# Optimization experiments

Hardware: AMD Instinct MI355X
Metric: run time of the kernel (lower is better)

The kernel has to match this reference:

```python
import jax, jax.numpy as jnp
import numpy as np

B, N, D = 4, 1024, 256
HEADS, LVLS, PTS, KSAMP = 8, 1, 4, 10
HF, WF, C = 200, 200, 256
HD = D // HEADS


def setup_inputs() -> dict:
    key = jax.random.key(0)
    ks = jax.random.split(key, 16)
    s = 0.02
    return {
        "query_embed": jax.random.normal(ks[0], (B, N, D), jnp.float32),
        # ctrl points in metric BEV coords (roughly inside pc_range)
        "ctrl_points": jax.random.normal(ks[1], (B, N, 4, 2), jnp.float32) * 30.0,
        "bev_features": jax.random.normal(ks[2], (B, C, HF, WF), jnp.float32),
        "spatial_shapes": jnp.array([[HF, WF]], jnp.int32),
        "pc_range": jnp.array([-51.2, -51.2, -5.0, 51.2, 51.2, 3.0], jnp.float32),
        # query_proj
        "W_q": jax.random.normal(ks[3], (D, D), jnp.float32) * s,
        "b_q": jnp.zeros((D,), jnp.float32),
        # MSDeformAttn.value_proj
        "W_val": jax.random.normal(ks[4], (D, D), jnp.float32) * s,
        "b_val": jnp.zeros((D,), jnp.float32),
        # MSDeformAttn.sampling_offsets  (D -> heads*levels*points*2)
        "W_off": jax.random.normal(ks[5], (D, HEADS * LVLS * PTS * 2), jnp.float32) * s,
        "b_off": jax.random.normal(ks[6], (HEADS * LVLS * PTS * 2,), jnp.float32) * 2.0,
        # MSDeformAttn.attention_weights (D -> heads*levels*points)
        "W_attn": jax.random.normal(ks[7], (D, HEADS * LVLS * PTS), jnp.float32) * s,
        "b_attn": jnp.zeros((HEADS * LVLS * PTS,), jnp.float32),
        # MSDeformAttn.output_proj
        "W_do": jax.random.normal(ks[8], (D, D), jnp.float32) * s,
        "b_do": jnp.zeros((D,), jnp.float32),
        # BezierDeformableAttention.output_proj
        "W_out": jax.random.normal(ks[9], (D, D), jnp.float32) * s,
        "b_out": jnp.zeros((D,), jnp.float32),
    }


def _forward(query_embed, ctrl_points, bev_features, pc_range,
             W_q, b_q, W_val, b_val, W_off, b_off, W_attn, b_attn,
             W_do, b_do, W_out, b_out):
    Bb, Nn = ctrl_points.shape[:2]
    _, Cc, Hh, Ww = bev_features.shape

    # ---- cubic Bezier interpolation: (B,N,4,2) -> (B,N,K,2) ----
    t = jnp.linspace(0.0, 1.0, KSAMP, dtype=query_embed.dtype)
    u = 1.0 - t
    coeff = jnp.stack([u ** 3, 3 * u ** 2 * t, 3 * u * t ** 2, t ** 3], axis=-1)  # (K,4)
    dense = jnp.einsum('kc,bncd->bnkd', coeff, ctrl_points)  # (B,N,K,2)

    # ---- normalize to [0,1] by pc_range, clamp ----
    lo = pc_range[:2]
    span = pc_range[3:5] - pc_range[:2]
    ref = jnp.clip((dense - lo) / span, 0.01, 0.99)  # (B,N,K,2)
    ref_center = ref.mean(axis=2)  # (B,N,2) -- center of the Bezier curve

    # ---- projections ----
    query = query_embed @ W_q + b_q  # (B,N,D)
    value = (bev_features.reshape(Bb, Cc, Hh * Ww).transpose(0, 2, 1) @ W_val + b_val)
    value = value.reshape(Bb, Hh * Ww, HEADS, HD)  # (B,HW,h,hd)

    offsets = (query @ W_off + b_off).reshape(Bb, Nn, HEADS, LVLS, PTS, 2)
    attn = (query @ W_attn + b_attn).reshape(Bb, Nn, HEADS, LVLS * PTS)
    attn = jax.nn.softmax(attn, axis=-1)  # (B,N,h,P)

    # sampling locations: ref (B,N,1(levels),2) + offsets/[W,H]
    norm = jnp.array([Ww, Hh], dtype=query.dtype)  # offset_normalizer (x=W, y=H)
    loc = ref_center[:, :, None, None, None, :] + offsets / norm  # (B,N,h,1,P,2)
    grid = 2.0 * loc[:, :, :, 0] - 1.0  # single level -> (B,N,h,P,2)

    # ---- bilinear grid_sample, align_corners=False, zero padding ----
    BH = Bb * HEADS
    val = value.transpose(0, 2, 3, 1).reshape(BH, HD, Hh * Ww)  # (BH,hd,HW)
    g = grid.transpose(0, 2, 1, 3, 4).reshape(BH, Nn, PTS, 2)  # (BH,N,P,2)
    x = (g[..., 0] + 1.0) * 0.5 * Ww - 0.5
    y = (g[..., 1] + 1.0) * 0.5 * Hh - 0.5
    x0 = jnp.floor(x).astype(jnp.int32); x1 = x0 + 1
    y0 = jnp.floor(y).astype(jnp.int32); y1 = y0 + 1
    wx = (x - x0).astype(val.dtype); wy = (y - y0).astype(val.dtype)

    def gather(yi, xi):
        valid = ((yi >= 0) & (yi < Hh) & (xi >= 0) & (xi < Ww))
        idx = jnp.clip(yi, 0, Hh - 1) * Ww + jnp.clip(xi, 0, Ww - 1)  # (BH,N,P)
        gv = jnp.take_along_axis(val, idx.reshape(BH, 1, Nn * PTS), axis=2)
        gv = gv.reshape(BH, HD, Nn, PTS)
        return gv * valid.astype(val.dtype)[:, None, :, :]

    sampled = (gather(y0, x0) * ((1 - wx) * (1 - wy))[:, None]
               + gather(y0, x1) * (wx * (1 - wy))[:, None]
               + gather(y1, x0) * ((1 - wx) * wy)[:, None]
               + gather(y1, x1) * (wx * wy)[:, None])  # (BH,hd,N,P)

    w = attn.transpose(0, 2, 1, 3).reshape(BH, 1, Nn, PTS)
    out = (sampled * w).sum(axis=-1)  # (BH,hd,N)
    out = out.reshape(Bb, HEADS * HD, Nn).transpose(0, 2, 1)  # (B,N,D)

    # mmcv MultiScaleDeformableAttention: output_proj + residual (identity = query)
    msda = out @ W_do + b_do + query
    return msda @ W_out + b_out


def reference(query_embed, ctrl_points, bev_features, spatial_shapes, pc_range,
              W_q, b_q, W_val, b_val, W_off, b_off, W_attn, b_attn,
              W_do, b_do, W_out, b_out):
    # spatial_shapes is recomputed from bev_features inside the torch module; unused here
    del spatial_shapes
    return _forward(query_embed, ctrl_points, bev_features, pc_range,
                    W_q, b_q, W_val, b_val, W_off, b_off, W_attn, b_attn,
                    W_do, b_do, W_out, b_out)
```

## Files before the change

kernel.cpp:

```cpp
#include <hip/hip_runtime.h>
#include <hip/hip_bf16.h>

#define BB 4
#define NN 1024
#define DD 256
#define NHEADS 8
#define NPTS 4
#define NKSAMP 10
#define HHF 200
#define WWF 200
#define HWF (HHF*WWF)

typedef __hip_bfloat16 bf16;

__device__ __forceinline__ float ldf(const float* p, size_t i){ return p[i]; }
__device__ __forceinline__ float ldf(const bf16*  p, size_t i){ return __bfloat162float(p[i]); }

__device__ __forceinline__ unsigned short f2bf(float f){
    unsigned u = __float_as_uint(f);
    return (unsigned short)((u + 0x7FFFu + ((u >> 16) & 1u)) >> 16);
}
__device__ __forceinline__ void load_bf16x8(const unsigned short* p, float* v){
    int4 t = *reinterpret_cast<const int4*>(p);
    unsigned q0 = (unsigned)t.x, q1 = (unsigned)t.y, q2 = (unsigned)t.z, q3 = (unsigned)t.w;
    v[0] = __uint_as_float(q0 << 16); v[1] = __uint_as_float(q0 & 0xFFFF0000u);
    v[2] = __uint_as_float(q1 << 16); v[3] = __uint_as_float(q1 & 0xFFFF0000u);
    v[4] = __uint_as_float(q2 << 16); v[5] = __uint_as_float(q2 & 0xFFFF0000u);
    v[6] = __uint_as_float(q3 << 16); v[7] = __uint_as_float(q3 & 0xFFFF0000u);
}
__device__ __forceinline__ void store_bf16x8(unsigned short* p, const float* v){
    int4 t;
    t.x = (int)((unsigned)f2bf(v[0]) | ((unsigned)f2bf(v[1]) << 16));
    t.y = (int)((unsigned)f2bf(v[2]) | ((unsigned)f2bf(v[3]) << 16));
    t.z = (int)((unsigned)f2bf(v[4]) | ((unsigned)f2bf(v[5]) << 16));
    t.w = (int)((unsigned)f2bf(v[6]) | ((unsigned)f2bf(v[7]) << 16));
    *reinterpret_cast<int4*>(p) = t;
}

__global__ void detect_kernel(const unsigned* __restrict__ pc_bits, int* __restrict__ flag){
    if (threadIdx.x == 0 && blockIdx.x == 0)
        *flag = (pc_bits[0] == 0xC24CCCCDu) ? 0 : 1;
}

template<typename T, int WANT>
__global__ __launch_bounds__(256) void transpose_kernel(const T* __restrict__ bev,
                                                        unsigned short* __restrict__ bevT,
                                                        const int* __restrict__ flag){
    if (*flag != WANT) return;
    __shared__ unsigned short tile[32][33];
    int b  = blockIdx.z;
    int c0 = blockIdx.y * 32;
    int p0 = blockIdx.x * 32;
    int tx = threadIdx.x & 31;
    int ty = threadIdx.x >> 5;
    const T* src = bev + (size_t)b * DD * HWF;
    #pragma unroll
    for (int i = 0; i < 4; i++){
        int c = c0 + ty + i*8;
        tile[ty + i*8][tx] = f2bf(ldf(src, (size_t)c * HWF + p0 + tx));
    }
    __syncthreads();
    unsigned short* dst = bevT + (size_t)b * HWF * DD;
    #pragma unroll
    for (int i = 0; i < 4; i++){
        int p = p0 + ty + i*8;
        dst[(size_t)p * DD + c0 + tx] = tile[tx][ty + i*8];
    }
}

template<int NT, int NM, bool ABF16, bool HEADSLICE, bool WSBIAS, bool RES, int WANT>
__global__ __launch_bounds__(256) void gemm_kernel(
    const void* __restrict__ Av, int lda,
    const float* __restrict__ B, int ldb,
    const float* __restrict__ bias,
    const float* __restrict__ wsb,
    const float* __restrict__ res,
    float* __restrict__ C, int ldc,
    const int* __restrict__ flag)
{
    if (*flag != WANT) return;
    __shared__ float As[256][68];
    const int n0  = blockIdx.x * NT;
    const int m0  = blockIdx.y * 64;
    const int tid = threadIdx.x;
    const int koff = HEADSLICE ? (n0 >> 5) * 256 : 0;

    if (ABF16){
        const unsigned short* A = (const unsigned short*)Av;
        int r  = tid >> 2;
        int kb = (tid & 3) * 8;
        #pragma unroll
        for (int kk = 0; kk < 8; kk++){
            int k = kb + kk*32;
            float v[8];
            load_bf16x8(A + (size_t)(m0 + r)*lda + koff + k, v);
            #pragma unroll
            for (int t = 0; t < 8; t++) As[k + t][r] = v[t];
        }
    } else {
        const float* A = (const float*)Av;
        int r  = tid >> 2;
        int kb = (tid & 3) * 4;
        #pragma unroll
        for (int kk = 0; kk < 16; kk++){
            int k = kb + kk*16;
            float4 v = *reinterpret_cast<const float4*>(A + (size_t)(m0 + r)*lda + k);
            As[k+0][r] = v.x; As[k+1][r] = v.y; As[k+2][r] = v.z; As[k+3][r] = v.w;
        }
    }
    __syncthreads();

    const int ti = tid & 15;
    const int tj = tid >> 4;
    float acc[4][NM];
    #pragma unroll
    for (int i = 0; i < 4; i++)
        #pragma unroll
        for (int j = 0; j < NM; j++) acc[i][j] = 0.f;

    const float* Bp = B + n0 + tj*NM;
    #pragma unroll 4
    for (int c = 0; c < 256; c++){
        float4 a = *reinterpret_cast<const float4*>(&As[c][ti*4]);
        float av[4] = {a.x, a.y, a.z, a.w};
        float bv[NM];
        if (NM == 4){
            float4 b4 = *reinterpret_cast<const float4*>(Bp + (size_t)c*ldb);
            bv[0] = b4.x; bv[1] = b4.y; bv[2] = b4.z; bv[3] = b4.w;
        } else {
            float2 b2 = *reinterpret_cast<const float2*>(Bp + (size_t)c*ldb);
            bv[0] = b2.x; bv[1] = b2.y;
        }
        #pragma unroll
        for (int i = 0; i < 4; i++)
            #pragma unroll
            for (int j = 0; j < NM; j++) acc[i][j] += av[i] * bv[j];
    }

    #pragma unroll
    for (int i = 0; i < 4; i++){
        int row = m0 + ti*4 + i;
        #pragma unroll
        for (int j = 0; j < NM; j++){
            int n = n0 + tj*NM + j;
            float bvv = bias[n];
            float v = acc[i][j] + (WSBIAS ? wsb[(size_t)row*8 + (n0 >> 5)]*bvv : bvv);
            if (RES) v += res[(size_t)row*256 + n];
            C[(size_t)row*ldc + n] = v;
        }
    }
}

template<int WANT>
__global__ __launch_bounds__(256) void coords_kernel(
    const float* __restrict__ ctrl, const float* __restrict__ pc,
    const float* __restrict__ oa,
    float* __restrict__ coords,
    float* __restrict__ wsb,
    const int* __restrict__ flag)
{
    if (*flag != WANT) return;
    const int m0 = blockIdx.x * 32;
    const int r  = threadIdx.x >> 3;
    const int h  = threadIdx.x & 7;
    const int m  = m0 + r;

    float cx[4], cy[4];
    #pragma unroll
    for (int i = 0; i < 4; i++){
        cx[i] = ctrl[(size_t)m*8 + i*2 + 0];
        cy[i] = ctrl[(size_t)m*8 + i*2 + 1];
    }
    float lox = pc[0], loy = pc[1];
    float spx = pc[3] - lox, spy = pc[4] - loy;
    float sx = 0.f, sy = 0.f;
    for (int k = 0; k < NKSAMP; k++){
        float t = (float)k / (float)(NKSAMP - 1);
        float u = 1.f - t;
        float c0 = u*u*u, c1 = 3.f*u*u*t, c2 = 3.f*u*t*t, c3 = t*t*t;
        float dx = c0*cx[0] + c1*cx[1] + c2*cx[2] + c3*cx[3];
        float dy = c0*cy[0] + c1*cy[1] + c2*cy[2] + c3*cy[3];
        float rx = fminf(fmaxf((dx - lox)/spx, 0.01f), 0.99f);
        float ry = fminf(fmaxf((dy - loy)/spy, 0.01f), 0.99f);
        sx += rx; sy += ry;
    }
    float cxp = (sx / (float)NKSAMP) * (float)WWF - 0.5f;
    float cyp = (sy / (float)NKSAMP) * (float)HHF - 0.5f;

    const float* row = oa + (size_t)m*96;
    float a0 = row[64 + h*4 + 0], a1 = row[64 + h*4 + 1];
    float a2 = row[64 + h*4 + 2], a3 = row[64 + h*4 + 3];
    float mx = fmaxf(fmaxf(a0, a1), fmaxf(a2, a3));
    float e0 = __expf(a0 - mx), e1 = __expf(a1 - mx);
    float e2 = __expf(a2 - mx), e3 = __expf(a3 - mx);
    float inv = 1.f / (e0 + e1 + e2 + e3);
    float wp[4] = {e0*inv, e1*inv, e2*inv, e3*inv};

    float* cp = coords + ((size_t)m*8 + h)*12;
    float wsum = 0.f;
    #pragma unroll
    for (int p = 0; p < 4; p++){
        float x = cxp + row[h*8 + p*2 + 0];
        float y = cyp + row[h*8 + p*2 + 1];
        cp[p*3 + 0] = x; cp[p*3 + 1] = y; cp[p*3 + 2] = wp[p];
        float fx = floorf(x), fy = floorf(y);
        int x0 = (int)fx, y0 = (int)fy;
        float wx = x - fx, wy = y - fy;
        bool vx0 = (unsigned)x0 < WWF, vx1 = (unsigned)(x0+1) < WWF;
        bool vy0 = (unsigned)y0 < HHF, vy1 = (unsigned)(y0+1) < HHF;
        float w = wp[p];
        if (vy0 && vx0) wsum += w*(1.f-wx)*(1.f-wy);
        if (vy0 && vx1) wsum += w*wx*(1.f-wy);
        if (vy1 && vx0) wsum += w*(1.f-wx)*wy;
        if (vy1 && vx1) wsum += w*wx*wy;
    }
    wsb[(size_t)m*8 + h] = wsum;
}

template<bool TRANS, int WANT>
__global__ __launch_bounds__(256) void gather_kernel(
    const unsigned short* __restrict__ bevT,
    const float* __restrict__ bev,
    const float* __restrict__ coords,
    unsigned short* __restrict__ g,
    const int* __restrict__ flag)
{
    if (*flag != WANT) return;
    const int m0  = blockIdx.x * 4;
    const int b   = m0 >> 10;
    const int sub = threadIdx.x & 31;
    const int grp = threadIdx.x >> 5;

    for (int it = 0; it < 4; it++){
        int rh = it*8 + grp;
        int m  = m0 + (rh >> 3);
        int h  = rh & 7;
        float acc[8] = {0.f,0.f,0.f,0.f,0.f,0.f,0.f,0.f};
        const float* cp = coords + ((size_t)m*8 + h)*12;

        #pragma unroll
        for (int p = 0; p < 4; p++){
            float x = cp[p*3+0], y = cp[p*3+1], w = cp[p*3+2];
            float fx = floorf(x), fy = floorf(y);
            int x0 = (int)fx, y0 = (int)fy;
            float wx = x - fx, wy = y - fy;
            int   xs[4] = {x0, x0+1, x0,   x0+1};
            int   ys[4] = {y0, y0,   y0+1, y0+1};
            float ws4[4] = {w*(1.f-wx)*(1.f-wy), w*wx*(1.f-wy), w*(1.f-wx)*wy, w*wx*wy};
            #pragma unroll
            for (int cidx = 0; cidx < 4; cidx++){
                int xi = xs[cidx], yi = ys[cidx];
                if ((unsigned)xi < WWF && (unsigned)yi < HHF){
                    float wgt = ws4[cidx];
                    if (TRANS){
                        const unsigned short* rowp =
                            bevT + (((size_t)b*HWF + yi*WWF + xi)*DD + sub*8);
                        float v[8]; load_bf16x8(rowp, v);
                        #pragma unroll
                        for (int i = 0; i < 8; i++) acc[i] += wgt * v[i];
                    } else {
                        size_t base = ((size_t)b*DD + sub*8)*HWF + (size_t)(yi*WWF + xi);
                        #pragma unroll
                        for (int i = 0; i < 8; i++) acc[i] += wgt * bev[base + (size_t)i*HWF];
                    }
                }
            }
        }
        store_bf16x8(g + ((size_t)m*2048 + h*256 + sub*8), acc);
    }
}

template<typename T, bool TRANS, int WANT>
__global__ __launch_bounds__(256) void monolith_kernel(
    const T* __restrict__ qe, const T* __restrict__ ctrl,
    const T* __restrict__ bev, const bf16* __restrict__ bevT,
    const T* __restrict__ pc,
    const T* __restrict__ Wq, const T* __restrict__ bq,
    const T* __restrict__ Wval, const T* __restrict__ bval,
    const T* __restrict__ Woff, const T* __restrict__ boff,
    const T* __restrict__ Wattn, const T* __restrict__ battn,
    const T* __restrict__ Wdo, const T* __restrict__ bdo,
    const T* __restrict__ Wout, const T* __restrict__ bout,
    float* __restrict__ out, const int* __restrict__ flag)
{
    if (*flag != WANT) return;
    __shared__ float qe_s[4][256];
    __shared__ float q_s[4][256];
    __shared__ float oa_s[4][96];
    __shared__ float cen_s[4][2];
    __shared__ int   sx0_s[4][32];
    __shared__ int   sy0_s[4][32];
    __shared__ float swx_s[4][32];
    __shared__ float swy_s[4][32];
    __shared__ float sww_s[4][32];
    __shared__ float ws_s[4][8];
    __shared__ float g_s[4][2048];
    __shared__ float t_s[4][256];

    const int m0  = blockIdx.x * 4;
    const int b   = m0 >> 10;
    const int tid = threadIdx.x;

    for (int i = tid; i < 4*256; i += 256){
        int r = i >> 8, c = i & 255;
        qe_s[r][c] = ldf(qe, (size_t)(m0 + r)*256 + c);
    }
    if (tid < 4){
        int r = tid;
        float cx[4], cy[4];
        #pragma unroll
        for (int i = 0; i < 4; i++){
            cx[i] = ldf(ctrl, (size_t)(m0+r)*8 + i*2 + 0);
            cy[i] = ldf(ctrl, (size_t)(m0+r)*8 + i*2 + 1);
        }
        float lox = ldf(pc,0), loy = ldf(pc,1);
        float spx = ldf(pc,3) - lox, spy = ldf(pc,4) - loy;
        float sx = 0.f, sy = 0.f;
        for (int k = 0; k < NKSAMP; k++){
            float t = (float)k / (float)(NKSAMP - 1);
            float u = 1.f - t;
            float c0 = u*u*u, c1 = 3.f*u*u*t, c2 = 3.f*u*t*t, c3 = t*t*t;
            float dx = c0*cx[0] + c1*cx[1] + c2*cx[2] + c3*cx[3];
            float dy = c0*cy[0] + c1*cy[1] + c2*cy[2] + c3*cy[3];
            float rx = fminf(fmaxf((dx - lox)/spx, 0.01f), 0.99f);
            float ry = fminf(fmaxf((dy - loy)/spy, 0.01f), 0.99f);
            sx += rx; sy += ry;
        }
        cen_s[r][0] = sx / (float)NKSAMP;
        cen_s[r][1] = sy / (float)NKSAMP;
    }
    __syncthreads();

    {
        const int j = tid;
        float acc[4] = {0.f, 0.f, 0.f, 0.f};
        for (int c = 0; c < 256; c++){
            float w = ldf(Wq, (size_t)c*256 + j);
            #pragma unroll
            for (int r = 0; r < 4; r++) acc[r] += qe_s[r][c] * w;
        }
        float bias = ldf(bq, j);
        #pragma unroll
        for (int r = 0; r < 4; r++) q_s[r][j] = acc[r] + bias;
    }
    __syncthreads();

    for (int idx = tid; idx < 4*96; idx += 256){
        int r = idx / 96, col = idx % 96;
        float acc = 0.f;
        if (col < 64){
            for (int c = 0; c < 256; c++) acc += q_s[r][c] * ldf(Woff, (size_t)c*64 + col);
            acc += ldf(boff, col);
        } else {
            int cc = col - 64;
            for (int c = 0; c < 256; c++) acc += q_s[r][c] * ldf(Wattn, (size_t)c*32 + cc);
            acc += ldf(battn, cc);
        }
        oa_s[r][col] = acc;
    }
    __syncthreads();

    if (tid < 32){
        int r = tid >> 3, h = tid & 7;
        float a0 = oa_s[r][64 + h*4 + 0], a1 = oa_s[r][64 + h*4 + 1];
        float a2 = oa_s[r][64 + h*4 + 2], a3 = oa_s[r][64 + h*4 + 3];
        float mx = fmaxf(fmaxf(a0, a1), fmaxf(a2, a3));
        float e0 = __expf(a0 - mx), e1 = __expf(a1 - mx);
        float e2 = __expf(a2 - mx), e3 = __expf(a3 - mx);
        float inv = 1.f / (e0 + e1 + e2 + e3);
        float wp[4] = {e0*inv, e1*inv, e2*inv, e3*inv};
        float cxp = cen_s[r][0] * (float)WWF - 0.5f;
        float cyp = cen_s[r][1] * (float)HHF - 0.5f;
        float wsum = 0.f;
        #pragma unroll
        for (int p = 0; p < 4; p++){
            float x = cxp + oa_s[r][h*8 + p*2 + 0];
            float y = cyp + oa_s[r][h*8 + p*2 + 1];
            float fx = floorf(x), fy = floorf(y);
            int x0 = (int)fx, y0 = (int)fy;
            float wx = x - fx, wy = y - fy;
            int s = h*4 + p;
            sx0_s[r][s] = x0; sy0_s[r][s] = y0;
            swx_s[r][s] = wx; swy_s[r][s] = wy;
            sww_s[r][s] = wp[p];
            bool vx0 = (unsigned)x0 < WWF, vx1 = (unsigned)(x0+1) < WWF;
            bool vy0 = (unsigned)y0 < HHF, vy1 = (unsigned)(y0+1) < HHF;
            float w = wp[p];
            if (vy0 && vx0) wsum += w*(1.f-wx)*(1.f-wy);
            if (vy0 && vx1) wsum += w*wx*(1.f-wy);
            if (vy1 && vx0) wsum += w*(1.f-wx)*wy;
            if (vy1 && vx1) wsum += w*wx*wy;
        }
        ws_s[r][h] = wsum;
    }
    __syncthreads();

    {
        const int c = tid;
        const bf16* baseT = bevT + (size_t)b * HWF * DD;
        const T*    baseR = bev  + (size_t)b * DD * HWF;
        for (int r = 0; r < 4; r++){
            #pragma unroll
            for (int h = 0; h < 8; h++){
                float acc = 0.f;
                #pragma unroll
                for (int p = 0; p < 4; p++){
                    int s = h*4 + p;
                    int x0 = sx0_s[r][s], y0 = sy0_s[r][s];
                    float wx = swx_s[r][s], wy = swy_s[r][s], w = sww_s[r][s];
                    float w00 = w*(1.f-wx)*(1.f-wy);
                    float w01 = w*wx*(1.f-wy);
                    float w10 = w*(1.f-wx)*wy;
                    float w11 = w*wx*wy;
                    bool vy0 = (unsigned)y0 < HHF, vy1 = (unsigned)(y0+1) < HHF;
                    bool vx0 = (unsigned)x0 < WWF, vx1 = (unsigned)(x0+1) < WWF;
                    if (vy0){
                        int rowp = y0*WWF + x0;
                        if (vx0) acc += w00 * (TRANS ? __bfloat162float(baseT[(size_t)rowp*DD + c])
                                                     : ldf(baseR, (size_t)c*HWF + rowp));
                        if (vx1) acc += w01 * (TRANS ? __bfloat162float(baseT[(size_t)(rowp+1)*DD + c])
                                                     : ldf(baseR, (size_t)c*HWF + rowp+1));
                    }
                    if (vy1){
                        int rowp = (y0+1)*WWF + x0;
                        if (vx0) acc += w10 * (TRANS ? __bfloat162float(baseT[(size_t)rowp*DD + c])
                                                     : ldf(baseR, (size_t)c*HWF + rowp));
                        if (vx1) acc += w11 * (TRANS ? __bfloat162float(baseT[(size_t)(rowp+1)*DD + c])
                                                     : ldf(baseR, (size_t)c*HWF + rowp+1));
                    }
                }
                g_s[r][h*256 + c] = acc;
            }
        }
    }
    __syncthreads();

    {
        const int j = tid;
        const int h = j >> 5;
        float acc[4] = {0.f, 0.f, 0.f, 0.f};
        for (int c = 0; c < 256; c++){
            float w = ldf(Wval, (size_t)c*256 + j);
            #pragma unroll
            for (int r = 0; r < 4; r++) acc[r] += g_s[r][h*256 + c] * w;
        }
        float bv = ldf(bval, j);
        #pragma unroll
        for (int r = 0; r < 4; r++) t_s[r][j] = acc[r] + ws_s[r][h] * bv;
    }
    __syncthreads();

    {
        const int j = tid;
        float acc[4] = {0.f, 0.f, 0.f, 0.f};
        for (int c = 0; c < 256; c++){
            float w = ldf(Wdo, (size_t)c*256 + j);
            #pragma unroll
            for (int r = 0; r < 4; r++) acc[r] += t_s[r][c] * w;
        }
        __syncthreads();
        float bd = ldf(bdo, j);
        #pragma unroll
        for (int r = 0; r < 4; r++) t_s[r][j] = acc[r] + bd + q_s[r][j];
    }
    __syncthreads();

    {
        const int j = tid;
        float acc[4] = {0.f, 0.f, 0.f, 0.f};
        for (int c = 0; c < 256; c++){
            float w = ldf(Wout, (size_t)c*256 + j);
            #pragma unroll
            for (int r = 0; r < 4; r++) acc[r] += t_s[r][c] * w;
        }
        float bo = ldf(bout, j);
        #pragma unroll
        for (int r = 0; r < 4; r++)
            out[(size_t)(m0+r)*256 + j] = acc[r] + bo;
    }
}

template<typename T, bool TRANS, int WANT>
static void launch_monolith(void* const* d_in, const bf16* bevT, float* out,
                            const int* flag, hipStream_t stream)
{
    monolith_kernel<T, TRANS, WANT><<<dim3(BB*NN/4), 256, 0, stream>>>(
        (const T*)d_in[0], (const T*)d_in[1], (const T*)d_in[2], bevT,
        (const T*)d_in[4],
        (const T*)d_in[5], (const T*)d_in[6], (const T*)d_in[7], (const T*)d_in[8],
        (const T*)d_in[9], (const T*)d_in[10], (const T*)d_in[11], (const T*)d_in[12],
        (const T*)d_in[13], (const T*)d_in[14], (const T*)d_in[15], (const T*)d_in[16],
        out, flag);
}

extern "C" void kernel_launch(void* const* d_in, const int* in_sizes, int n_in,
                              void* d_out, int out_size, void* d_ws, size_t ws_size,
                              hipStream_t stream)
{
    (void)in_sizes; (void)n_in; (void)out_size;
    float* out = (float*)d_out;
    char*  ws  = (char*)d_ws;

    const size_t OF_FLAG = 0;
    const size_t OF_QBUF = 256;
    const size_t OF_OA   = OF_QBUF + (size_t)4096*256*4;
    const size_t OF_CO   = OF_OA   + (size_t)4096*96*4;
    const size_t OF_WSB  = OF_CO   + (size_t)4096*8*48;
    const size_t OF_T1   = OF_WSB  + (size_t)4096*8*4;
    const size_t OF_T2   = OF_T1   + (size_t)4096*256*4;
    const size_t OF_G    = OF_T2   + (size_t)4096*256*4;
    const size_t OF_BT   = OF_G    + (size_t)4096*2048*2;
    const size_t NEED_A  = OF_BT + (size_t)BB*HWF*DD*2;
    const size_t NEED_R4 = 64 + (size_t)BB*HWF*DD*2;
    const size_t NEED_B  = OF_BT;

    int*            flag   = (int*)(ws + OF_FLAG);
    float*          qbuf   = (float*)(ws + OF_QBUF);
    float*          oa     = (float*)(ws + OF_OA);
    float*          coords = (float*)(ws + OF_CO);
    float*          wsb    = (float*)(ws + OF_WSB);
    float*          t1     = (float*)(ws + OF_T1);
    float*          t2     = (float*)(ws + OF_T2);
    unsigned short* g      = (unsigned short*)(ws + OF_G);
    unsigned short* bevT   = (unsigned short*)(ws + OF_BT);

    const float* qe    = (const float*)d_in[0];
    const float* ctrl  = (const float*)d_in[1];
    const float* bev   = (const float*)d_in[2];
    const float* pc    = (const float*)d_in[4];
    const float* Wq    = (const float*)d_in[5];
    const float* bq    = (const float*)d_in[6];
    const float* Wval  = (const float*)d_in[7];
    const float* bval  = (const float*)d_in[8];
    const float* Woff  = (const float*)d_in[9];
    const float* boff  = (const float*)d_in[10];
    const float* Wattn = (const float*)d_in[11];
    const float* battn = (const float*)d_in[12];
    const float* Wdo   = (const float*)d_in[13];
    const float* bdo   = (const float*)d_in[14];
    const float* Wout  = (const float*)d_in[15];
    const float* bout  = (const float*)d_in[16];

    detect_kernel<<<1, 64, 0, stream>>>((const unsigned*)d_in[4], flag);

    if (ws_size >= NEED_A || ws_size >= NEED_B){
        const bool haveT = (ws_size >= NEED_A);

        if (haveT)
            transpose_kernel<float, 0><<<dim3(HWF/32, DD/32, BB), 256, 0, stream>>>(
                bev, bevT, flag);

        gemm_kernel<64,4,false,false,false,false,0><<<dim3(4,64), 256, 0, stream>>>(
            qe, 256, Wq, 256, bq, nullptr, nullptr, qbuf, 256, flag);
        gemm_kernel<64,4,false,false,false,false,0><<<dim3(1,64), 256, 0, stream>>>(
            qbuf, 256, Woff, 64, boff, nullptr, nullptr, oa, 96, flag);
        gemm_kernel<32,2,false,false,false,false,0><<<dim3(1,64), 256, 0, stream>>>(
            qbuf, 256, Wattn, 32, battn, nullptr, nullptr, oa + 64, 96, flag);
        coords_kernel<0><<<dim3(128), 256, 0, stream>>>(ctrl, pc, oa, coords, wsb, flag);
        if (haveT)
            gather_kernel<true, 0><<<dim3(1024), 256, 0, stream>>>(bevT, bev, coords, g, flag);
        else
            gather_kernel<false,0><<<dim3(1024), 256, 0, stream>>>(bevT, bev, coords, g, flag);
        gemm_kernel<32,2,true,true,true,false,0><<<dim3(8,64), 256, 0, stream>>>(
            g, 2048, Wval, 256, bval, wsb, nullptr, t1, 256, flag);
        gemm_kernel<64,4,false,false,false,true,0><<<dim3(4,64), 256, 0, stream>>>(
            t1, 256, Wdo, 256, bdo, nullptr, qbuf, t2, 256, flag);
        gemm_kernel<64,4,false,false,false,false,0><<<dim3(4,64), 256, 0, stream>>>(
            t2, 256, Wout, 256, bout, nullptr, nullptr, out, 256, flag);

        if (haveT){
            transpose_kernel<bf16, 1><<<dim3(HWF/32, DD/32, BB), 256, 0, stream>>>(
                (const bf16*)d_in[2], bevT, flag);
            launch_monolith<bf16, true, 1>(d_in, (const bf16*)bevT, out, flag, stream);
        } else {
            launch_monolith<bf16, false, 1>(d_in, (const bf16*)bevT, out, flag, stream);
        }
    } else if (ws_size >= NEED_R4){
        bf16* bevT4 = (bf16*)(ws + 64);
        transpose_kernel<float, 0><<<dim3(HWF/32, DD/32, BB), 256, 0, stream>>>(
            bev, (unsigned short*)bevT4, flag);
        transpose_kernel<bf16, 1><<<dim3(HWF/32, DD/32, BB), 256, 0, stream>>>(
            (const bf16*)d_in[2], (unsigned short*)bevT4, flag);
        launch_monolith<float, true, 0>(d_in, bevT4, out, flag, stream);
        launch_monolith<bf16,  true, 1>(d_in, bevT4, out, flag, stream);
    } else {
        launch_monolith<float, false, 0>(d_in, (const bf16*)ws, out, flag, stream);
        launch_monolith<bf16,  false, 1>(d_in, (const bf16*)ws, out, flag, stream);
    }
}
```

Baseline: 533.1 us.

## Fuse offset/attention projections with coords kernel and drop the runtime dtype dispatch

Merges the sampling-offset GEMM, the attention-weight GEMM and the coordinate/softmax computation into one kernel that keeps the projection results in shared memory. This removes the intermediate buffer and two launches. It also deletes the flag-based runtime detection and the bf16 fallback path, including the monolith kernel and the flag-gated launches that used to exit early. GEMM epilogue stores become float4/float2 vector writes. In exchange, the fused kernel runs on only 64 blocks, and the code now supports only float32 inputs with the full workspace layout.

```diff
diff --git a/kernel.cpp b/kernel.cpp
--- a/kernel.cpp
+++ b/kernel.cpp
@@ -13,9 +13,6 @@
 
 typedef __hip_bfloat16 bf16;
 
-__device__ __forceinline__ float ldf(const float* p, size_t i){ return p[i]; }
-__device__ __forceinline__ float ldf(const bf16*  p, size_t i){ return __bfloat162float(p[i]); }
-
 __device__ __forceinline__ unsigned short f2bf(float f){
     unsigned u = __float_as_uint(f);
     return (unsigned short)((u + 0x7FFFu + ((u >> 16) & 1u)) >> 16);
@@ -37,27 +34,19 @@
     *reinterpret_cast<int4*>(p) = t;
 }
 
-__global__ void detect_kernel(const unsigned* __restrict__ pc_bits, int* __restrict__ flag){
-    if (threadIdx.x == 0 && blockIdx.x == 0)
-        *flag = (pc_bits[0] == 0xC24CCCCDu) ? 0 : 1;
-}
-
-template<typename T, int WANT>
-__global__ __launch_bounds__(256) void transpose_kernel(const T* __restrict__ bev,
-                                                        unsigned short* __restrict__ bevT,
-                                                        const int* __restrict__ flag){
-    if (*flag != WANT) return;
+__global__ __launch_bounds__(256) void transpose_kernel(const float* __restrict__ bev,
+                                                        unsigned short* __restrict__ bevT){
     __shared__ unsigned short tile[32][33];
     int b  = blockIdx.z;
     int c0 = blockIdx.y * 32;
     int p0 = blockIdx.x * 32;
     int tx = threadIdx.x & 31;
     int ty = threadIdx.x >> 5;
-    const T* src = bev + (size_t)b * DD * HWF;
+    const float* src = bev + (size_t)b * DD * HWF;
     #pragma unroll
     for (int i = 0; i < 4; i++){
         int c = c0 + ty + i*8;
-        tile[ty + i*8][tx] = f2bf(ldf(src, (size_t)c * HWF + p0 + tx));
+        tile[ty + i*8][tx] = f2bf(src[(size_t)c * HWF + p0 + tx]);
     }
     __syncthreads();
     unsigned short* dst = bevT + (size_t)b * HWF * DD;
@@ -68,17 +57,15 @@
     }
 }
 
-template<int NT, int NM, bool ABF16, bool HEADSLICE, bool WSBIAS, bool RES, int WANT>
+template<int NT, int NM, bool ABF16, bool HEADSLICE, bool WSBIAS, bool RES>
 __global__ __launch_bounds__(256) void gemm_kernel(
     const void* __restrict__ Av, int lda,
     const float* __restrict__ B, int ldb,
     const float* __restrict__ bias,
     const float* __restrict__ wsb,
     const float* __restrict__ res,
-    float* __restrict__ C, int ldc,
-    const int* __restrict__ flag)
+    float* __restrict__ C, int ldc)
 {
-    if (*flag != WANT) return;
     __shared__ float As[256][68];
     const int n0  = blockIdx.x * NT;
     const int m0  = blockIdx.y * 64;
@@ -140,92 +127,157 @@
     #pragma unroll
     for (int i = 0; i < 4; i++){
         int row = m0 + ti*4 + i;
-        #pragma unroll
-        for (int j = 0; j < NM; j++){
-            int n = n0 + tj*NM + j;
-            float bvv = bias[n];
-            float v = acc[i][j] + (WSBIAS ? wsb[(size_t)row*8 + (n0 >> 5)]*bvv : bvv);
-            if (RES) v += res[(size_t)row*256 + n];
-            C[(size_t)row*ldc + n] = v;
-        }
-    }
-}
-
-template<int WANT>
-__global__ __launch_bounds__(256) void coords_kernel(
-    const float* __restrict__ ctrl, const float* __restrict__ pc,
-    const float* __restrict__ oa,
+        float wsv = WSBIAS ? wsb[(size_t)row*8 + (n0 >> 5)] : 0.f;
+        if (NM == 4){
+            float4 v; float* vp = (float*)&v;
+            #pragma unroll
+            for (int j = 0; j < 4; j++){
+                int n = n0 + tj*4 + j;
+                float bvv = bias[n];
+                float t = acc[i][j] + (WSBIAS ? wsv*bvv : bvv);
+                if (RES) t += res[(size_t)row*256 + n];
+                vp[j] = t;
+            }
+            *reinterpret_cast<float4*>(&C[(size_t)row*ldc + n0 + tj*4]) = v;
+        } else {
+            float2 v; float* vp = (float*)&v;
+            #pragma unroll
+            for (int j = 0; j < 2; j++){
+                int n = n0 + tj*2 + j;
+                float bvv = bias[n];
+                float t = acc[i][j] + (WSBIAS ? wsv*bvv : bvv);
+                if (RES) t += res[(size_t)row*256 + n];
+                vp[j] = t;
+            }
+            *reinterpret_cast<float2*>(&C[(size_t)row*ldc + n0 + tj*2]) = v;
+        }
+    }
+}
+
+__global__ __launch_bounds__(256) void oacoords_kernel(
+    const float* __restrict__ Q, const float* __restrict__ ctrl, const float* __restrict__ pc,
+    const float* __restrict__ Woff, const float* __restrict__ boff,
+    const float* __restrict__ Wattn, const float* __restrict__ battn,
     float* __restrict__ coords,
-    float* __restrict__ wsb,
-    const int* __restrict__ flag)
+    float* __restrict__ wsb)
 {
-    if (*flag != WANT) return;
-    const int m0 = blockIdx.x * 32;
-    const int r  = threadIdx.x >> 3;
-    const int h  = threadIdx.x & 7;
-    const int m  = m0 + r;
-
-    float cx[4], cy[4];
-    #pragma unroll
-    for (int i = 0; i < 4; i++){
-        cx[i] = ctrl[(size_t)m*8 + i*2 + 0];
-        cy[i] = ctrl[(size_t)m*8 + i*2 + 1];
-    }
-    float lox = pc[0], loy = pc[1];
-    float spx = pc[3] - lox, spy = pc[4] - loy;
-    float sx = 0.f, sy = 0.f;
-    for (int k = 0; k < NKSAMP; k++){
-        float t = (float)k / (float)(NKSAMP - 1);
-        float u = 1.f - t;
-        float c0 = u*u*u, c1 = 3.f*u*u*t, c2 = 3.f*u*t*t, c3 = t*t*t;
-        float dx = c0*cx[0] + c1*cx[1] + c2*cx[2] + c3*cx[3];
-        float dy = c0*cy[0] + c1*cy[1] + c2*cy[2] + c3*cy[3];
-        float rx = fminf(fmaxf((dx - lox)/spx, 0.01f), 0.99f);
-        float ry = fminf(fmaxf((dy - loy)/spy, 0.01f), 0.99f);
-        sx += rx; sy += ry;
-    }
-    float cxp = (sx / (float)NKSAMP) * (float)WWF - 0.5f;
-    float cyp = (sy / (float)NKSAMP) * (float)HHF - 0.5f;
-
-    const float* row = oa + (size_t)m*96;
-    float a0 = row[64 + h*4 + 0], a1 = row[64 + h*4 + 1];
-    float a2 = row[64 + h*4 + 2], a3 = row[64 + h*4 + 3];
-    float mx = fmaxf(fmaxf(a0, a1), fmaxf(a2, a3));
-    float e0 = __expf(a0 - mx), e1 = __expf(a1 - mx);
-    float e2 = __expf(a2 - mx), e3 = __expf(a3 - mx);
-    float inv = 1.f / (e0 + e1 + e2 + e3);
-    float wp[4] = {e0*inv, e1*inv, e2*inv, e3*inv};
-
-    float* cp = coords + ((size_t)m*8 + h)*12;
-    float wsum = 0.f;
-    #pragma unroll
-    for (int p = 0; p < 4; p++){
-        float x = cxp + row[h*8 + p*2 + 0];
-        float y = cyp + row[h*8 + p*2 + 1];
-        cp[p*3 + 0] = x; cp[p*3 + 1] = y; cp[p*3 + 2] = wp[p];
-        float fx = floorf(x), fy = floorf(y);
-        int x0 = (int)fx, y0 = (int)fy;
-        float wx = x - fx, wy = y - fy;
-        bool vx0 = (unsigned)x0 < WWF, vx1 = (unsigned)(x0+1) < WWF;
-        bool vy0 = (unsigned)y0 < HHF, vy1 = (unsigned)(y0+1) < HHF;
-        float w = wp[p];
-        if (vy0 && vx0) wsum += w*(1.f-wx)*(1.f-wy);
-        if (vy0 && vx1) wsum += w*wx*(1.f-wy);
-        if (vy1 && vx0) wsum += w*(1.f-wx)*wy;
-        if (vy1 && vx1) wsum += w*wx*wy;
-    }
-    wsb[(size_t)m*8 + h] = wsum;
-}
-
-template<bool TRANS, int WANT>
+    __shared__ __align__(16) char smem[256*68*4];
+    float (*As)[68] = (float(*)[68])smem;
+    __shared__ float cen_s[64][2];
+    const int m0  = blockIdx.x * 64;
+    const int tid = threadIdx.x;
+
+    {
+        int r  = tid >> 2;
+        int kb = (tid & 3) * 4;
+        #pragma unroll
+        for (int kk = 0; kk < 16; kk++){
+            int k = kb + kk*16;
+            float4 v = *reinterpret_cast<const float4*>(Q + (size_t)(m0 + r)*256 + k);
+            As[k+0][r] = v.x; As[k+1][r] = v.y; As[k+2][r] = v.z; As[k+3][r] = v.w;
+        }
+    }
+    if (tid < 64){
+        int m = m0 + tid;
+        float cx[4], cy[4];
+        #pragma unroll
+        for (int i = 0; i < 4; i++){
+            cx[i] = ctrl[(size_t)m*8 + i*2 + 0];
+            cy[i] = ctrl[(size_t)m*8 + i*2 + 1];
+        }
+        float lox = pc[0], loy = pc[1];
+        float spx = pc[3] - lox, spy = pc[4] - loy;
+        float sx = 0.f, sy = 0.f;
+        for (int k = 0; k < NKSAMP; k++){
+            float t = (float)k / (float)(NKSAMP - 1);
+            float u = 1.f - t;
+            float c0 = u*u*u, c1 = 3.f*u*u*t, c2 = 3.f*u*t*t, c3 = t*t*t;
+            float dx = c0*cx[0] + c1*cx[1] + c2*cx[2] + c3*cx[3];
+            float dy = c0*cy[0] + c1*cy[1] + c2*cy[2] + c3*cy[3];
+            float rx = fminf(fmaxf((dx - lox)/spx, 0.01f), 0.99f);
+            float ry = fminf(fmaxf((dy - loy)/spy, 0.01f), 0.99f);
+            sx += rx; sy += ry;
+        }
+        cen_s[tid][0] = (sx / (float)NKSAMP) * (float)WWF - 0.5f;
+        cen_s[tid][1] = (sy / (float)NKSAMP) * (float)HHF - 0.5f;
+    }
+    __syncthreads();
+
+    const int ti = tid & 15;
+    const int tj = tid >> 4;
+    float ao[4][4], aa[4][2];
+    #pragma unroll
+    for (int i = 0; i < 4; i++){
+        #pragma unroll
+        for (int j = 0; j < 4; j++) ao[i][j] = 0.f;
+        aa[i][0] = 0.f; aa[i][1] = 0.f;
+    }
+    #pragma unroll 4
+    for (int c = 0; c < 256; c++){
+        float4 a = *reinterpret_cast<const float4*>(&As[c][ti*4]);
+        float av[4] = {a.x, a.y, a.z, a.w};
+        float4 bo = *reinterpret_cast<const float4*>(Woff + (size_t)c*64 + tj*4);
+        float2 ba = *reinterpret_cast<const float2*>(Wattn + (size_t)c*32 + tj*2);
+        #pragma unroll
+        for (int i = 0; i < 4; i++){
+            ao[i][0] += av[i]*bo.x; ao[i][1] += av[i]*bo.y;
+            ao[i][2] += av[i]*bo.z; ao[i][3] += av[i]*bo.w;
+            aa[i][0] += av[i]*ba.x; aa[i][1] += av[i]*ba.y;
+        }
+    }
+    __syncthreads();
+    float* oaS = (float*)smem;
+    #pragma unroll
+    for (int i = 0; i < 4; i++){
+        int r = ti*4 + i;
+        #pragma unroll
+        for (int j = 0; j < 4; j++) oaS[r*96 + tj*4 + j] = ao[i][j] + boff[tj*4 + j];
+        oaS[r*96 + 64 + tj*2 + 0] = aa[i][0] + battn[tj*2 + 0];
+        oaS[r*96 + 64 + tj*2 + 1] = aa[i][1] + battn[tj*2 + 1];
+    }
+    __syncthreads();
+
+    for (int idx = tid; idx < 512; idx += 256){
+        int r = idx >> 3, h = idx & 7;
+        int m = m0 + r;
+        const float* row = oaS + r*96;
+        float a0 = row[64 + h*4 + 0], a1 = row[64 + h*4 + 1];
+        float a2 = row[64 + h*4 + 2], a3 = row[64 + h*4 + 3];
+        float mx = fmaxf(fmaxf(a0, a1), fmaxf(a2, a3));
+        float e0 = __expf(a0 - mx), e1 = __expf(a1 - mx);
+        float e2 = __expf(a2 - mx), e3 = __expf(a3 - mx);
+        float inv = 1.f / (e0 + e1 + e2 + e3);
+        float wp[4] = {e0*inv, e1*inv, e2*inv, e3*inv};
+        float cxp = cen_s[r][0], cyp = cen_s[r][1];
+        float* cp = coords + ((size_t)m*8 + h)*12;
+        float wsum = 0.f;
+        #pragma unroll
+        for (int p = 0; p < 4; p++){
+            float x = cxp + row[h*8 + p*2 + 0];
+            float y = cyp + row[h*8 + p*2 + 1];
+            cp[p*3 + 0] = x; cp[p*3 + 1] = y; cp[p*3 + 2] = wp[p];
+            float fx = floorf(x), fy = floorf(y);
+            int x0 = (int)fx, y0 = (int)fy;
+            float wx = x - fx, wy = y - fy;
+            bool vx0 = (unsigned)x0 < WWF, vx1 = (unsigned)(x0+1) < WWF;
+            bool vy0 = (unsigned)y0 < HHF, vy1 = (unsigned)(y0+1) < HHF;
+            float w = wp[p];
+            if (vy0 && vx0) wsum += w*(1.f-wx)*(1.f-wy);
+            if (vy0 && vx1) wsum += w*wx*(1.f-wy);
+            if (vy1 && vx0) wsum += w*(1.f-wx)*wy;
+            if (vy1 && vx1) wsum += w*wx*wy;
+        }
+        wsb[(size_t)m*8 + h] = wsum;
+    }
+}
+
+template<bool TRANS>
 __global__ __launch_bounds__(256) void gather_kernel(
     const unsigned short* __restrict__ bevT,
     const float* __restrict__ bev,
     const float* __restrict__ coords,
-    unsigned short* __restrict__ g,
-    const int* __restrict__ flag)
+    unsigned short* __restrict__ g)
 {
-    if (*flag != WANT) return;
     const int m0  = blockIdx.x * 4;
     const int b   = m0 >> 10;
     const int sub = threadIdx.x & 31;
@@ -244,8 +296,8 @@
             float fx = floorf(x), fy = floorf(y);
             int x0 = (int)fx, y0 = (int)fy;
             float wx = x - fx, wy = y - fy;
-            int   xs[4] = {x0, x0+1, x0,   x0+1};
-            int   ys[4] = {y0, y0,   y0+1, y0+1};
+            int   xs[4]  = {x0, x0+1, x0,   x0+1};
+            int   ys[4]  = {y0, y0,   y0+1, y0+1};
             float ws4[4] = {w*(1.f-wx)*(1.f-wy), w*wx*(1.f-wy), w*(1.f-wx)*wy, w*wx*wy};
             #pragma unroll
             for (int cidx = 0; cidx < 4; cidx++){
@@ -270,229 +322,6 @@
     }
 }
 
-template<typename T, bool TRANS, int WANT>
-__global__ __launch_bounds__(256) void monolith_kernel(
-    const T* __restrict__ qe, const T* __restrict__ ctrl,
-    const T* __restrict__ bev, const bf16* __restrict__ bevT,
-    const T* __restrict__ pc,
-    const T* __restrict__ Wq, const T* __restrict__ bq,
-    const T* __restrict__ Wval, const T* __restrict__ bval,
-    const T* __restrict__ Woff, const T* __restrict__ boff,
-    const T* __restrict__ Wattn, const T* __restrict__ battn,
-    const T* __restrict__ Wdo, const T* __restrict__ bdo,
-    const T* __restrict__ Wout, const T* __restrict__ bout,
-    float* __restrict__ out, const int* __restrict__ flag)
-{
-    if (*flag != WANT) return;
-    __shared__ float qe_s[4][256];
-    __shared__ float q_s[4][256];
-    __shared__ float oa_s[4][96];
-    __shared__ float cen_s[4][2];
-    __shared__ int   sx0_s[4][32];
-    __shared__ int   sy0_s[4][32];
-    __shared__ float swx_s[4][32];
-    __shared__ float swy_s[4][32];
-    __shared__ float sww_s[4][32];
-    __shared__ float ws_s[4][8];
-    __shared__ float g_s[4][2048];
-    __shared__ float t_s[4][256];
-
-    const int m0  = blockIdx.x * 4;
-    const int b   = m0 >> 10;
-    const int tid = threadIdx.x;
-
-    for (int i = tid; i < 4*256; i += 256){
-        int r = i >> 8, c = i & 255;
-        qe_s[r][c] = ldf(qe, (size_t)(m0 + r)*256 + c);
-    }
-    if (tid < 4){
-        int r = tid;
-        float cx[4], cy[4];
-        #pragma unroll
-        for (int i = 0; i < 4; i++){
-            cx[i] = ldf(ctrl, (size_t)(m0+r)*8 + i*2 + 0);
-            cy[i] = ldf(ctrl, (size_t)(m0+r)*8 + i*2 + 1);
-        }
-        float lox = ldf(pc,0), loy = ldf(pc,1);
-        float spx = ldf(pc,3) - lox, spy = ldf(pc,4) - loy;
-        float sx = 0.f, sy = 0.f;
-        for (int k = 0; k < NKSAMP; k++){
-            float t = (float)k / (float)(NKSAMP - 1);
-            float u = 1.f - t;
-            float c0 = u*u*u, c1 = 3.f*u*u*t, c2 = 3.f*u*t*t, c3 = t*t*t;
-            float dx = c0*cx[0] + c1*cx[1] + c2*cx[2] + c3*cx[3];
-            float dy = c0*cy[0] + c1*cy[1] + c2*cy[2] + c3*cy[3];
-            float rx = fminf(fmaxf((dx - lox)/spx, 0.01f), 0.99f);
-            float ry = fminf(fmaxf((dy - loy)/spy, 0.01f), 0.99f);
-            sx += rx; sy += ry;
-        }
-        cen_s[r][0] = sx / (float)NKSAMP;
-        cen_s[r][1] = sy / (float)NKSAMP;
-    }
-    __syncthreads();
-
-    {
-        const int j = tid;
-        float acc[4] = {0.f, 0.f, 0.f, 0.f};
-        for (int c = 0; c < 256; c++){
-            float w = ldf(Wq, (size_t)c*256 + j);
-            #pragma unroll
-            for (int r = 0; r < 4; r++) acc[r] += qe_s[r][c] * w;
-        }
-        float bias = ldf(bq, j);
-        #pragma unroll
-        for (int r = 0; r < 4; r++) q_s[r][j] = acc[r] + bias;
-    }
-    __syncthreads();
-
-    for (int idx = tid; idx < 4*96; idx += 256){
-        int r = idx / 96, col = idx % 96;
-        float acc = 0.f;
-        if (col < 64){
-            for (int c = 0; c < 256; c++) acc += q_s[r][c] * ldf(Woff, (size_t)c*64 + col);
-            acc += ldf(boff, col);
-        } else {
-            int cc = col - 64;
-            for (int c = 0; c < 256; c++) acc += q_s[r][c] * ldf(Wattn, (size_t)c*32 + cc);
-            acc += ldf(battn, cc);
-        }
-        oa_s[r][col] = acc;
-    }
-    __syncthreads();
-
-    if (tid < 32){
-        int r = tid >> 3, h = tid & 7;
-        float a0 = oa_s[r][64 + h*4 + 0], a1 = oa_s[r][64 + h*4 + 1];
-        float a2 = oa_s[r][64 + h*4 + 2], a3 = oa_s[r][64 + h*4 + 3];
-        float mx = fmaxf(fmaxf(a0, a1), fmaxf(a2, a3));
-        float e0 = __expf(a0 - mx), e1 = __expf(a1 - mx);
-        float e2 = __expf(a2 - mx), e3 = __expf(a3 - mx);
-        float inv = 1.f / (e0 + e1 + e2 + e3);
-        float wp[4] = {e0*inv, e1*inv, e2*inv, e3*inv};
-        float cxp = cen_s[r][0] * (float)WWF - 0.5f;
-        float cyp = cen_s[r][1] * (float)HHF - 0.5f;
-        float wsum = 0.f;
-        #pragma unroll
-        for (int p = 0; p < 4; p++){
-            float x = cxp + oa_s[r][h*8 + p*2 + 0];
-            float y = cyp + oa_s[r][h*8 + p*2 + 1];
-            float fx = floorf(x), fy = floorf(y);
-            int x0 = (int)fx, y0 = (int)fy;
-            float wx = x - fx, wy = y - fy;
-            int s = h*4 + p;
-            sx0_s[r][s] = x0; sy0_s[r][s] = y0;
-            swx_s[r][s] = wx; swy_s[r][s] = wy;
-            sww_s[r][s] = wp[p];
-            bool vx0 = (unsigned)x0 < WWF, vx1 = (unsigned)(x0+1) < WWF;
-            bool vy0 = (unsigned)y0 < HHF, vy1 = (unsigned)(y0+1) < HHF;
-            float w = wp[p];
-            if (vy0 && vx0) wsum += w*(1.f-wx)*(1.f-wy);
-            if (vy0 && vx1) wsum += w*wx*(1.f-wy);
-            if (vy1 && vx0) wsum += w*(1.f-wx)*wy;
-            if (vy1 && vx1) wsum += w*wx*wy;
-        }
-        ws_s[r][h] = wsum;
-    }
-    __syncthreads();
-
-    {
-        const int c = tid;
-        const bf16* baseT = bevT + (size_t)b * HWF * DD;
-        const T*    baseR = bev  + (size_t)b * DD * HWF;
-        for (int r = 0; r < 4; r++){
-            #pragma unroll
-            for (int h = 0; h < 8; h++){
-                float acc = 0.f;
-                #pragma unroll
-                for (int p = 0; p < 4; p++){
-                    int s = h*4 + p;
-                    int x0 = sx0_s[r][s], y0 = sy0_s[r][s];
-                    float wx = swx_s[r][s], wy = swy_s[r][s], w = sww_s[r][s];
-                    float w00 = w*(1.f-wx)*(1.f-wy);
-                    float w01 = w*wx*(1.f-wy);
-                    float w10 = w*(1.f-wx)*wy;
-                    float w11 = w*wx*wy;
-                    bool vy0 = (unsigned)y0 < HHF, vy1 = (unsigned)(y0+1) < HHF;
-                    bool vx0 = (unsigned)x0 < WWF, vx1 = (unsigned)(x0+1) < WWF;
-                    if (vy0){
-                        int rowp = y0*WWF + x0;
-                        if (vx0) acc += w00 * (TRANS ? __bfloat162float(baseT[(size_t)rowp*DD + c])
-                                                     : ldf(baseR, (size_t)c*HWF + rowp));
-                        if (vx1) acc += w01 * (TRANS ? __bfloat162float(baseT[(size_t)(rowp+1)*DD + c])
-                                                     : ldf(baseR, (size_t)c*HWF + rowp+1));
-                    }
-                    if (vy1){
-                        int rowp = (y0+1)*WWF + x0;
-                        if (vx0) acc += w10 * (TRANS ? __bfloat162float(baseT[(size_t)rowp*DD + c])
-                                                     : ldf(baseR, (size_t)c*HWF + rowp));
-                        if (vx1) acc += w11 * (TRANS ? __bfloat162float(baseT[(size_t)(rowp+1)*DD + c])
-                                                     : ldf(baseR, (size_t)c*HWF + rowp+1));
-                    }
-                }
-                g_s[r][h*256 + c] = acc;
-            }
-        }
-    }
-    __syncthreads();
-
-    {
-        const int j = tid;
-        const int h = j >> 5;
-        float acc[4] = {0.f, 0.f, 0.f, 0.f};
-        for (int c = 0; c < 256; c++){
-            float w = ldf(Wval, (size_t)c*256 + j);
-            #pragma unroll
-            for (int r = 0; r < 4; r++) acc[r] += g_s[r][h*256 + c] * w;
-        }
-        float bv = ldf(bval, j);
-        #pragma unroll
-        for (int r = 0; r < 4; r++) t_s[r][j] = acc[r] + ws_s[r][h] * bv;
-    }
-    __syncthreads();
-
-    {
-        const int j = tid;
-        float acc[4] = {0.f, 0.f, 0.f, 0.f};
-        for (int c = 0; c < 256; c++){
-            float w = ldf(Wdo, (size_t)c*256 + j);
-            #pragma unroll
-            for (int r = 0; r < 4; r++) acc[r] += t_s[r][c] * w;
-        }
-        __syncthreads();
-        float bd = ldf(bdo, j);
-        #pragma unroll
-        for (int r = 0; r < 4; r++) t_s[r][j] = acc[r] + bd + q_s[r][j];
-    }
-    __syncthreads();
-
-    {
-        const int j = tid;
-        float acc[4] = {0.f, 0.f, 0.f, 0.f};
-        for (int c = 0; c < 256; c++){
-            float w = ldf(Wout, (size_t)c*256 + j);
-            #pragma unroll
-            for (int r = 0; r < 4; r++) acc[r] += t_s[r][c] * w;
-        }
-        float bo = ldf(bout, j);
-        #pragma unroll
-        for (int r = 0; r < 4; r++)
-            out[(size_t)(m0+r)*256 + j] = acc[r] + bo;
-    }
-}
-
-template<typename T, bool TRANS, int WANT>
-static void launch_monolith(void* const* d_in, const bf16* bevT, float* out,
-                            const int* flag, hipStream_t stream)
-{
-    monolith_kernel<T, TRANS, WANT><<<dim3(BB*NN/4), 256, 0, stream>>>(
-        (const T*)d_in[0], (const T*)d_in[1], (const T*)d_in[2], bevT,
-        (const T*)d_in[4],
-        (const T*)d_in[5], (const T*)d_in[6], (const T*)d_in[7], (const T*)d_in[8],
-        (const T*)d_in[9], (const T*)d_in[10], (const T*)d_in[11], (const T*)d_in[12],
-        (const T*)d_in[13], (const T*)d_in[14], (const T*)d_in[15], (const T*)d_in[16],
-        out, flag);
-}
-
 extern "C" void kernel_launch(void* const* d_in, const int* in_sizes, int n_in,
                               void* d_out, int out_size, void* d_ws, size_t ws_size,
                               hipStream_t stream)
@@ -501,22 +330,16 @@
     float* out = (float*)d_out;
     char*  ws  = (char*)d_ws;
 
-    const size_t OF_FLAG = 0;
-    const size_t OF_QBUF = 256;
-    const size_t OF_OA   = OF_QBUF + (size_t)4096*256*4;
-    const size_t OF_CO   = OF_OA   + (size_t)4096*96*4;
+    const size_t OF_QBUF = 0;
+    const size_t OF_CO   = OF_QBUF + (size_t)4096*256*4;
     const size_t OF_WSB  = OF_CO   + (size_t)4096*8*48;
     const size_t OF_T1   = OF_WSB  + (size_t)4096*8*4;
     const size_t OF_T2   = OF_T1   + (size_t)4096*256*4;
     const size_t OF_G    = OF_T2   + (size_t)4096*256*4;
     const size_t OF_BT   = OF_G    + (size_t)4096*2048*2;
-    const size_t NEED_A  = OF_BT + (size_t)BB*HWF*DD*2;
-    const size_t NEED_R4 = 64 + (size_t)BB*HWF*DD*2;
-    const size_t NEED_B  = OF_BT;
-
-    int*            flag   = (int*)(ws + OF_FLAG);
+    const size_t NEED    = OF_BT   + (size_t)BB*HWF*DD*2;
+
     float*          qbuf   = (float*)(ws + OF_QBUF);
-    float*          oa     = (float*)(ws + OF_OA);
     float*          coords = (float*)(ws + OF_CO);
     float*          wsb    = (float*)(ws + OF_WSB);
     float*          t1     = (float*)(ws + OF_T1);
@@ -541,50 +364,23 @@
     const float* Wout  = (const float*)d_in[15];
     const float* bout  = (const float*)d_in[16];
 
-    detect_kernel<<<1, 64, 0, stream>>>((const unsigned*)d_in[4], flag);
-
-    if (ws_size >= NEED_A || ws_size >= NEED_B){
-        const bool haveT = (ws_size >= NEED_A);
-
-        if (haveT)
-            transpose_kernel<float, 0><<<dim3(HWF/32, DD/32, BB), 256, 0, stream>>>(
-                bev, bevT, flag);
-
-        gemm_kernel<64,4,false,false,false,false,0><<<dim3(4,64), 256, 0, stream>>>(
-            qe, 256, Wq, 256, bq, nullptr, nullptr, qbuf, 256, flag);
-        gemm_kernel<64,4,false,false,false,false,0><<<dim3(1,64), 256, 0, stream>>>(
-            qbuf, 256, Woff, 64, boff, nullptr, nullptr, oa, 96, flag);
-        gemm_kernel<32,2,false,false,false,false,0><<<dim3(1,64), 256, 0, stream>>>(
-            qbuf, 256, Wattn, 32, battn, nullptr, nullptr, oa + 64, 96, flag);
-        coords_kernel<0><<<dim3(128), 256, 0, stream>>>(ctrl, pc, oa, coords, wsb, flag);
-        if (haveT)
-            gather_kernel<true, 0><<<dim3(1024), 256, 0, stream>>>(bevT, bev, coords, g, flag);
-        else
-            gather_kernel<false,0><<<dim3(1024), 256, 0, stream>>>(bevT, bev, coords, g, flag);
-        gemm_kernel<32,2,true,true,true,false,0><<<dim3(8,64), 256, 0, stream>>>(
-            g, 2048, Wval, 256, bval, wsb, nullptr, t1, 256, flag);
-        gemm_kernel<64,4,false,false,false,true,0><<<dim3(4,64), 256, 0, stream>>>(
-            t1, 256, Wdo, 256, bdo, nullptr, qbuf, t2, 256, flag);
-        gemm_kernel<64,4,false,false,false,false,0><<<dim3(4,64), 256, 0, stream>>>(
-            t2, 256, Wout, 256, bout, nullptr, nullptr, out, 256, flag);
-
-        if (haveT){
-            transpose_kernel<bf16, 1><<<dim3(HWF/32, DD/32, BB), 256, 0, stream>>>(
-                (const bf16*)d_in[2], bevT, flag);
-            launch_monolith<bf16, true, 1>(d_in, (const bf16*)bevT, out, flag, stream);
-        } else {
-            launch_monolith<bf16, false, 1>(d_in, (const bf16*)bevT, out, flag, stream);
-        }
-    } else if (ws_size >= NEED_R4){
-        bf16* bevT4 = (bf16*)(ws + 64);
-        transpose_kernel<float, 0><<<dim3(HWF/32, DD/32, BB), 256, 0, stream>>>(
-            bev, (unsigned short*)bevT4, flag);
-        transpose_kernel<bf16, 1><<<dim3(HWF/32, DD/32, BB), 256, 0, stream>>>(
-            (const bf16*)d_in[2], (unsigned short*)bevT4, flag);
-        launch_monolith<float, true, 0>(d_in, bevT4, out, flag, stream);
-        launch_monolith<bf16,  true, 1>(d_in, bevT4, out, flag, stream);
-    } else {
-        launch_monolith<float, false, 0>(d_in, (const bf16*)ws, out, flag, stream);
-        launch_monolith<bf16,  false, 1>(d_in, (const bf16*)ws, out, flag, stream);
-    }
-}
+    const bool haveT = (ws_size >= NEED);
+
+    if (haveT)
+        transpose_kernel<<<dim3(HWF/32, DD/32, BB), 256, 0, stream>>>(bev, bevT);
+
+    gemm_kernel<64,4,false,false,false,false><<<dim3(4,64), 256, 0, stream>>>(
+        qe, 256, Wq, 256, bq, nullptr, nullptr, qbuf, 256);
+    oacoords_kernel<<<dim3(64), 256, 0, stream>>>(
+        qbuf, ctrl, pc, Woff, boff, Wattn, battn, coords, wsb);
+    if (haveT)
+        gather_kernel<true ><<<dim3(1024), 256, 0, stream>>>(bevT, bev, coords, g);
+    else
+        gather_kernel<false><<<dim3(1024), 256, 0, stream>>>(bevT, bev, coords, g);
+    gemm_kernel<32,2,true,true,true,false><<<dim3(8,64), 256, 0, stream>>>(
+        g, 2048, Wval, 256, bval, wsb, nullptr, t1, 256);
+    gemm_kernel<64,4,false,false,false,true><<<dim3(4,64), 256, 0, stream>>>(
+        t1, 256, Wdo, 256, bdo, nullptr, qbuf, t2, 256);
+    gemm_kernel<64,4,false,false,false,false><<<dim3(4,64), 256, 0, stream>>>(
+        t2, 256, Wout, 256, bout, nullptr, nullptr, out, 256);
+}
```

Measured after the change: 489.3 us. 8.2% less time.
